# Kernel optimization log

Hardware: AMD Instinct MI355X
Metric: run time of the kernel (lower is better)

The kernel has to match this reference:

```python
import jax, jax.numpy as jnp
import numpy as np

H, NH, HD = 1024, 16, 64
WIN = 256
W = WIN // 2  # one-sided window
EXP = 4
PAD_VAL = 0.0  # pad_token_id
B, S0 = 2, 2048
NEG = float(np.finfo(np.float32).min)


def setup_inputs() -> dict:
    key = jax.random.key(0)
    ks = jax.random.split(key, 12)

    def lin(k, fi, fo):
        k1, k2 = jax.random.split(k)
        w = jax.random.normal(k1, (fi, fo), jnp.float32) / np.float32(np.sqrt(fi))
        b = jax.random.normal(k2, (fo,), jnp.float32) * 0.02
        return w, b

    x = jax.random.normal(ks[0], (B, S0, H), jnp.float32)
    mask = jnp.zeros((B, S0), jnp.int32)  # 0 = real token, 1 = pad
    wq, bq = lin(ks[1], H, H)
    wk, bk = lin(ks[2], H, H)
    wv, bv = lin(ks[3], H, H)
    wqg, bqg = lin(ks[4], H, H)
    wkg, bkg = lin(ks[5], H, H)
    wvg, bvg = lin(ks[6], H, H)
    ln_g = jnp.ones((H,), jnp.float32)
    ln_b = jnp.zeros((H,), jnp.float32)
    w1, b1 = lin(ks[7], H, H * EXP)
    w2, b2 = lin(ks[8], H * EXP, H)
    return dict(x=x, mask=mask, wq=wq, bq=bq, wk=wk, bk=bk, wv=wv, bv=bv,
                wqg=wqg, bqg=bqg, wkg=wkg, bkg=bkg, wvg=wvg, bvg=bvg,
                ln_g=ln_g, ln_b=ln_b, w1=w1, b1=b1, w2=w2, b2=b2)


def _forward(x, mask, wq, bq, wk, bk, wv, bv, wqg, bqg, wkg, bkg, wvg, bvg,
             ln_g, ln_b, w1, b1, w2, b2):
    Bsz, s0, _ = x.shape
    pad = WIN - s0 % WIN
    xp = jnp.pad(x, ((0, 0), (0, pad), (0, 0)), constant_values=PAD_VAL)
    m = jnp.pad(mask, ((0, 0), (0, pad)), constant_values=1)
    S = s0 + pad
    lm = (m * -10000).at[:, -1].set(10000)  # [B,S]; task='cls': last token global
    is_masked = lm < 0
    remove = lm != 0  # masked OR global keys removed from local windows

    inv_sqrt = np.float32(1.0 / np.sqrt(HD))
    q = ((xp @ wq + bq) * inv_sqrt).reshape(Bsz, S, NH, HD)
    k = (xp @ wk + bk).reshape(Bsz, S, NH, HD)
    v = (xp @ wv + bv).reshape(Bsz, S, NH, HD)

    nc = S // W
    # chunked banded scores: query chunk of W attends to 3W keys (prev/self/next)
    qc = q.transpose(0, 2, 1, 3).reshape(Bsz, NH, nc, W, HD)
    kpad = jnp.pad(k.transpose(0, 2, 1, 3), ((0, 0), (0, 0), (W, W), (0, 0)))
    idx3w = jnp.arange(nc)[:, None] * W + jnp.arange(3 * W)[None, :]  # [nc,3W]
    kc = kpad[:, :, idx3w]  # [B,NH,nc,3W,HD]
    sc = jnp.einsum('bhcpd,bhckd->bhcpk', qc, kc)  # [B,NH,nc,W,3W]
    p_idx = jnp.arange(W)[:, None]
    d_idx = jnp.arange(2 * W + 1)[None, :]
    band = sc[:, :, :, p_idx, p_idx + d_idx]  # [B,NH,nc,W,2W+1]
    band = band.reshape(Bsz, NH, S, 2 * W + 1).transpose(0, 2, 1, 3)  # [B,S,NH,2W+1]

    # key index j = i + d - W for offset d in [0, 2W]
    j = jnp.arange(S)[:, None] + jnp.arange(2 * W + 1)[None, :] - W
    in_range = (j >= 0) & (j < S)
    jc = jnp.clip(j, 0, S - 1)
    fmask = jnp.where(remove, NEG, 0.0)  # [B,S]
    band = band + fmask[:, jc][:, :, None, :]
    band = jnp.where(in_range[None, :, None, :], band, -jnp.inf)

    # global key column (single global token = last position), concatenated in front
    gcol = jnp.einsum('bshd,bhd->bsh', q, k[:, -1])[..., None]  # [B,S,NH,1]
    scores = jnp.concatenate([gcol, band], axis=-1)  # [B,S,NH,2W+2]
    probs = jax.nn.softmax(scores, axis=-1)
    probs = jnp.where(is_masked[:, :, None, None], 0.0, probs)

    out_g = probs[..., 0][..., None] * v[:, -1][:, None]  # [B,S,NH,HD]
    lp = probs[..., 1:].transpose(0, 2, 1, 3).reshape(Bsz, NH, nc, W, 2 * W + 1)
    pc = jnp.zeros((Bsz, NH, nc, W, 3 * W), probs.dtype).at[:, :, :, p_idx, p_idx + d_idx].set(lp)
    vpad = jnp.pad(v.transpose(0, 2, 1, 3), ((0, 0), (0, 0), (W, W), (0, 0)))
    vc = vpad[:, :, idx3w]  # [B,NH,nc,3W,HD]
    out_l = jnp.einsum('bhcpk,bhckd->bhcpd', pc, vc).reshape(Bsz, NH, S, HD).transpose(0, 2, 1, 3)
    attn = (out_l + out_g).reshape(Bsz, S, H)

    # full global attention for the global token (separate projections)
    qg = ((xp[:, -1] @ wqg + bqg) * inv_sqrt).reshape(Bsz, NH, HD)
    kg = (xp @ wkg + bkg).reshape(Bsz, S, NH, HD)
    vg = (xp @ wvg + bvg).reshape(Bsz, S, NH, HD)
    gs = jnp.einsum('bhd,bshd->bhs', qg, kg)
    gs = jnp.where(is_masked[:, None, :], NEG, gs)
    gout = jnp.einsum('bhs,bshd->bhd', jax.nn.softmax(gs, axis=-1), vg).reshape(Bsz, H)
    attn = attn.at[:, -1].set(gout)

    y = (xp + attn)[:, :s0]  # residual then strip padding
    mu = y.mean(-1, keepdims=True)
    var = ((y - mu) ** 2).mean(-1, keepdims=True)
    y = (y - mu) * jax.lax.rsqrt(var + 1e-5) * ln_g + ln_b
    h = jax.nn.gelu(y @ w1 + b1, approximate=False)
    return y + (h @ w2 + b2)


def reference(x, mask, wq, bq, wk, bk, wv, bv, wqg, bqg, wkg, bkg, wvg, bvg,
              ln_g, ln_b, w1, b1, w2, b2):
    return _forward(x, mask, wq, bq, wk, bk, wv, bv, wqg, bqg, wkg, bkg,
                    wvg, bvg, ln_g, ln_b, w1, b1, w2, b2)
```

## Files before the change

kernel.cpp:

```cpp
#include <hip/hip_runtime.h>


using bf16x8 = __attribute__((ext_vector_type(8))) short;
using bf16x4 = __attribute__((ext_vector_type(4))) short;
using f32x4  = __attribute__((ext_vector_type(4))) float;

__device__ __forceinline__ float b2f(short s) {
    return __uint_as_float(((unsigned int)(unsigned short)s) << 16);
}
__device__ __forceinline__ short f2b(float f) {
    unsigned int u = __float_as_uint(f);
    u += 0x7fffu + ((u >> 16) & 1u);
    return (short)(u >> 16);
}
__device__ __forceinline__ f32x4 mfma16(bf16x8 a, bf16x8 b, f32x4 c) {
    return __builtin_amdgcn_mfma_f32_16x16x32_bf16(a, b, c, 0, 0, 0);
}
__device__ __forceinline__ float safe_exp(float x) {
    return expf((x <= 0.f) ? x : 0.f);
}
__device__ __forceinline__ void load_lds16(const short* g, short* l) {
    __builtin_amdgcn_global_load_lds((const __attribute__((address_space(1))) void*)g,
                                     (__attribute__((address_space(3))) void*)l, 16, 0, 0);
}
#define NEGF (-3.0e38f)

__global__ void cvt_f32_bf16(const float* __restrict__ in, short* __restrict__ out, int n) {
    int i = (blockIdx.x * 256 + threadIdx.x) * 4;
    f32x4 v = *(const f32x4*)(in + i);
    bf16x4 o;
#pragma unroll
    for (int j = 0; j < 4; ++j) o[j] = f2b(v[j]);
    *(bf16x4*)(out + i) = o;
}

__global__ void cvt_transpose(const float* __restrict__ in, short* __restrict__ out,
                              int R, int C) {
    __shared__ short tile[32][33];
    int bx = blockIdx.x * 32, by = blockIdx.y * 32;
    int tx = threadIdx.x, ty = threadIdx.y;
    for (int i = ty; i < 32; i += 8)
        tile[i][tx] = f2b(in[(size_t)(by + i) * C + bx + tx]);
    __syncthreads();
    for (int i = ty; i < 32; i += 8)
        out[(size_t)(bx + i) * R + by + tx] = tile[tx][i];
}

__global__ void cvt_transpose_qkv(const float* __restrict__ wq, const float* __restrict__ wk,
                                  const float* __restrict__ wv, short* __restrict__ out) {
    __shared__ short tile[32][33];
    const float* in = (blockIdx.z == 0) ? wq : (blockIdx.z == 1) ? wk : wv;
    short* dst = out + (size_t)blockIdx.z * 1024 * 1024;
    int bx = blockIdx.x * 32, by = blockIdx.y * 32;
    int tx = threadIdx.x, ty = threadIdx.y;
    for (int i = ty; i < 32; i += 8)
        tile[i][tx] = f2b(in[(size_t)(by + i) * 1024 + bx + tx]);
    __syncthreads();
    for (int i = ty; i < 32; i += 8)
        dst[(size_t)(bx + i) * 1024 + by + tx] = tile[tx][i];
}

__global__ __launch_bounds__(256, 3) void gemm_bt(
    const short* __restrict__ A, const short* __restrict__ Bt,
    const float* __restrict__ bias0, const float* __restrict__ bias1,
    const float* __restrict__ bias2,
    short* __restrict__ C, short* __restrict__ Vt,
    int M, int N, int K, float scale, int mode)
{
    __shared__ short As[128 * 64];
    __shared__ short Bs[128 * 64];
    int m0 = blockIdx.x * 128, n0 = blockIdx.y * 128;
    int t = threadIdx.x;
    int wave = t >> 6, lane = t & 63, quad = lane >> 4, l16 = lane & 15;
    int wr = (wave >> 1) * 64, wc = (wave & 1) * 64;

    const short* ap[4]; const short* bp[4]; short* la[4]; short* lb[4];
    int gk = (((lane & 7) ^ (lane >> 3)) * 8);
#pragma unroll
    for (int l = 0; l < 4; ++l) {
        int c = wave * 4 + l;
        int row = c * 8 + (lane >> 3);
        ap[l] = A  + (size_t)(m0 + row) * K + gk;
        bp[l] = Bt + (size_t)(n0 + row) * K + gk;
        la[l] = As + c * 512;
        lb[l] = Bs + c * 512;
    }
    int sw = l16 & 7;

    f32x4 acc[4][4] = {};
    for (int k0 = 0; k0 < K; k0 += 64) {
#pragma unroll
        for (int l = 0; l < 4; ++l) { load_lds16(ap[l] + k0, la[l]); load_lds16(bp[l] + k0, lb[l]); }
        __syncthreads();
#pragma unroll
        for (int ks = 0; ks < 2; ++ks) {
            int slot = ((ks * 4 + quad) ^ sw) * 8;
            bf16x8 af[4], bfr[4];
#pragma unroll
            for (int i = 0; i < 4; ++i)
                af[i] = *(bf16x8*)(As + (wr + i * 16 + l16) * 64 + slot);
#pragma unroll
            for (int j = 0; j < 4; ++j)
                bfr[j] = *(bf16x8*)(Bs + (wc + j * 16 + l16) * 64 + slot);
#pragma unroll
            for (int i = 0; i < 4; ++i)
#pragma unroll
                for (int j = 0; j < 4; ++j)
                    acc[i][j] = mfma16(af[i], bfr[j], acc[i][j]);
        }
        __syncthreads();
    }

#pragma unroll
    for (int j = 0; j < 4; ++j) {
        int col = n0 + wc + j * 16 + l16;
        if (mode == 1) {
            float bs = bias0[col];
#pragma unroll
            for (int i = 0; i < 4; ++i) {
#pragma unroll
                for (int r = 0; r < 4; ++r) {
                    int row = m0 + wr + i * 16 + quad * 4 + r;
                    float v = acc[i][j][r] + bs;
                    v = 0.5f * v * (1.0f + erff(v * 0.70710678118f));
                    C[(size_t)row * N + col] = f2b(v);
                }
            }
        } else {
            int seg = col >> 10;
            const float* bpt = (seg == 0) ? bias0 : (seg == 1) ? bias1 : bias2;
            float bs = bpt[col & 1023];
            if (seg < 2) {
                float sc = (seg == 0) ? scale : 1.0f;
#pragma unroll
                for (int i = 0; i < 4; ++i)
#pragma unroll
                    for (int r = 0; r < 4; ++r) {
                        int row = m0 + wr + i * 16 + quad * 4 + r;
                        C[(size_t)row * N + col] = f2b((acc[i][j][r] + bs) * sc);
                    }
            } else {
                int h = (col >> 6) & 15, d = col & 63;
#pragma unroll
                for (int i = 0; i < 4; ++i) {
                    int row0 = m0 + wr + i * 16 + quad * 4;
                    int bb = row0 >> 11, s0 = row0 & 2047;
                    bf16x4 vv;
#pragma unroll
                    for (int r = 0; r < 4; ++r) vv[r] = f2b(acc[i][j][r] + bs);
                    *(bf16x4*)(Vt + (((size_t)(bb * 16 + h)) * 64 + d) * 2048 + s0) = vv;
                }
            }
        }
    }
}

__global__ __launch_bounds__(256, 4) void gemm64_bt(
    const short* __restrict__ A, const short* __restrict__ Bt,
    const float* __restrict__ bias, const float* __restrict__ resf,
    float* __restrict__ Cf, int M, int N, int K)
{
    __shared__ short As[64 * 64];
    __shared__ short Bs[64 * 64];
    int m0 = blockIdx.x * 64, n0 = blockIdx.y * 64;
    int t = threadIdx.x;
    int wave = t >> 6, lane = t & 63, quad = lane >> 4, l16 = lane & 15;
    int wr = (wave >> 1) * 32, wc = (wave & 1) * 32;

    const short* ap[2]; const short* bp[2]; short* la[2]; short* lb[2];
    int gk = (((lane & 7) ^ (lane >> 3)) * 8);
#pragma unroll
    for (int l = 0; l < 2; ++l) {
        int c = wave * 2 + l;
        int row = c * 8 + (lane >> 3);
        ap[l] = A  + (size_t)(m0 + row) * K + gk;
        bp[l] = Bt + (size_t)(n0 + row) * K + gk;
        la[l] = As + c * 512;
        lb[l] = Bs + c * 512;
    }
    int sw = l16 & 7;

    f32x4 acc[2][2] = {};
    for (int k0 = 0; k0 < K; k0 += 64) {
#pragma unroll
        for (int l = 0; l < 2; ++l) { load_lds16(ap[l] + k0, la[l]); load_lds16(bp[l] + k0, lb[l]); }
        __syncthreads();
#pragma unroll
        for (int ks = 0; ks < 2; ++ks) {
            int slot = ((ks * 4 + quad) ^ sw) * 8;
            bf16x8 af[2], bfr[2];
#pragma unroll
            for (int i = 0; i < 2; ++i)
                af[i] = *(bf16x8*)(As + (wr + i * 16 + l16) * 64 + slot);
#pragma unroll
            for (int j = 0; j < 2; ++j)
                bfr[j] = *(bf16x8*)(Bs + (wc + j * 16 + l16) * 64 + slot);
#pragma unroll
            for (int i = 0; i < 2; ++i)
#pragma unroll
                for (int j = 0; j < 2; ++j)
                    acc[i][j] = mfma16(af[i], bfr[j], acc[i][j]);
        }
        __syncthreads();
    }
#pragma unroll
    for (int j = 0; j < 2; ++j) {
        int col = n0 + wc + j * 16 + l16;
        float bs = bias[col];
#pragma unroll
        for (int i = 0; i < 2; ++i) {
#pragma unroll
            for (int r = 0; r < 4; ++r) {
                int row = m0 + wr + i * 16 + quad * 4 + r;
                Cf[(size_t)row * N + col] = acc[i][j][r] + bs + resf[(size_t)row * N + col];
            }
        }
    }
}

__global__ __launch_bounds__(256, 2) void attn_kernel(
    const short* __restrict__ QKV, const short* __restrict__ Vt,
    const int* __restrict__ mask,
    const float* __restrict__ bk, const float* __restrict__ bv,
    short* __restrict__ attn)
{
    extern __shared__ char smem[];
    short* PsQ = (short*)smem;
    short* KV  = (short*)(smem + 34816);
    float* gkf = (float*)(smem + 53248);
    float* gvf = (float*)(smem + 53504);

    int blk = blockIdx.x;
    int c = blk & 15, h = (blk >> 4) & 15, b = blk >> 8;
    int t = threadIdx.x;
    int wave = t >> 6, lane = t & 63, quad = lane >> 4, l16 = lane & 15;
    int q0 = c * 128;
    const int bs_off = b * 2048;
    const short* Q = QKV + h * 64;
    const short* K = QKV + 1024 + h * 64;

#pragma unroll
    for (int l = 0; l < 4; ++l) {
        int idx = l * 256 + t;
        int p = idx >> 3, dc = (idx & 7) * 8;
        *(bf16x8*)(PsQ + p * 72 + dc) =
            *(const bf16x8*)(Q + ((size_t)(bs_off + q0 + p)) * 3072 + dc);
    }
    if (t < 64) { gkf[t] = bk[h * 64 + t]; gvf[t] = bv[h * 64 + t]; }
    __syncthreads();

    bf16x8 aq[2][2];
#pragma unroll
    for (int ti = 0; ti < 2; ++ti)
#pragma unroll
        for (int ks = 0; ks < 2; ++ks)
            aq[ti][ks] = *(bf16x8*)(PsQ + (wave * 32 + ti * 16 + l16) * 72 + ks * 32 + quad * 8);

    float s_g[2][4];
#pragma unroll
    for (int ti = 0; ti < 2; ++ti)
#pragma unroll
        for (int r = 0; r < 4; ++r) {
            int row = wave * 32 + ti * 16 + quad * 4 + r;
            float part = 0.f;
#pragma unroll
            for (int dd = 0; dd < 4; ++dd) {
                int d = l16 * 4 + dd;
                part += b2f(PsQ[row * 72 + d]) * gkf[d];
            }
#pragma unroll
            for (int dsh = 1; dsh < 16; dsh <<= 1) part += __shfl_xor(part, dsh);
            s_g[ti][r] = part;
        }

    f32x4 o_acc[2][4] = {};
    float m_run[2][4], l_run[2][4];
#pragma unroll
    for (int ti = 0; ti < 2; ++ti)
#pragma unroll
        for (int r = 0; r < 4; ++r) { m_run[ti][r] = NEGF; l_run[ti][r] = 0.f; }

    int kt_beg = (q0 == 0) ? 1 : 0;
    int kt_end = (q0 + 256 > 2048) ? 2 : 3;
    for (int kt = kt_beg; kt < kt_end; ++kt) {
        int jb = q0 + (kt - 1) * 128;
        __syncthreads();
#pragma unroll
        for (int l = 0; l < 4; ++l) {
            int idx = l * 256 + t;
            int p = idx >> 3, dc = (idx & 7) * 8;
            *(bf16x8*)(KV + p * 72 + dc) =
                *(const bf16x8*)(K + ((size_t)(bs_off + jb + p)) * 3072 + dc);
        }
        __syncthreads();

        f32x4 s_acc[2][8] = {};
#pragma unroll
        for (int ks = 0; ks < 2; ++ks) {
            bf16x8 bk8[8];
#pragma unroll
            for (int tj = 0; tj < 8; ++tj)
                bk8[tj] = *(bf16x8*)(KV + (tj * 16 + l16) * 72 + ks * 32 + quad * 8);
#pragma unroll
            for (int ti = 0; ti < 2; ++ti)
#pragma unroll
                for (int tj = 0; tj < 8; ++tj)
                    s_acc[ti][tj] = mfma16(aq[ti][ks], bk8[tj], s_acc[ti][tj]);
        }

        float negj[8]; int jcol[8];
#pragma unroll
        for (int tj = 0; tj < 8; ++tj) {
            jcol[tj] = jb + tj * 16 + l16;
            negj[tj] = (mask[bs_off + jcol[tj]] != 0) ? NEGF : 0.f;
        }
        float tmax[2][4];
#pragma unroll
        for (int ti = 0; ti < 2; ++ti)
#pragma unroll
            for (int r = 0; r < 4; ++r) tmax[ti][r] = NEGF;
#pragma unroll
        for (int ti = 0; ti < 2; ++ti) {
            int irow_base = q0 + wave * 32 + ti * 16 + quad * 4;
#pragma unroll
            for (int tj = 0; tj < 8; ++tj)
#pragma unroll
                for (int r = 0; r < 4; ++r) {
                    int dj = jcol[tj] - (irow_base + r);
                    float sc = (dj >= -128 && dj <= 128) ? (s_acc[ti][tj][r] + negj[tj]) : NEGF;
                    s_acc[ti][tj][r] = sc;
                    tmax[ti][r] = fmaxf(tmax[ti][r], sc);
                }
        }
#pragma unroll
        for (int ti = 0; ti < 2; ++ti)
#pragma unroll
            for (int r = 0; r < 4; ++r)
#pragma unroll
                for (int dsh = 1; dsh < 16; dsh <<= 1)
                    tmax[ti][r] = fmaxf(tmax[ti][r], __shfl_xor(tmax[ti][r], dsh));

        float alpha[2][4], lsum[2][4];
#pragma unroll
        for (int ti = 0; ti < 2; ++ti)
#pragma unroll
            for (int r = 0; r < 4; ++r) {
                float mnew = fmaxf(m_run[ti][r], tmax[ti][r]);
                alpha[ti][r] = safe_exp(m_run[ti][r] - mnew);
                m_run[ti][r] = mnew;
                lsum[ti][r] = 0.f;
            }
#pragma unroll
        for (int ti = 0; ti < 2; ++ti)
#pragma unroll
            for (int tj = 0; tj < 8; ++tj)
#pragma unroll
                for (int r = 0; r < 4; ++r) {
                    float p = safe_exp(s_acc[ti][tj][r] - m_run[ti][r]);
                    lsum[ti][r] += p;
                    PsQ[(wave * 32 + ti * 16 + quad * 4 + r) * 136 + tj * 16 + l16] = f2b(p);
                }
#pragma unroll
        for (int ti = 0; ti < 2; ++ti)
#pragma unroll
            for (int r = 0; r < 4; ++r) {
#pragma unroll
                for (int dsh = 1; dsh < 16; dsh <<= 1) lsum[ti][r] += __shfl_xor(lsum[ti][r], dsh);
                l_run[ti][r] = l_run[ti][r] * alpha[ti][r] + lsum[ti][r];
            }
#pragma unroll
        for (int ti = 0; ti < 2; ++ti)
#pragma unroll
            for (int dj = 0; dj < 4; ++dj)
#pragma unroll
                for (int r = 0; r < 4; ++r) o_acc[ti][dj][r] *= alpha[ti][r];

        __syncthreads();
#pragma unroll
        for (int l = 0; l < 4; ++l) {
            int idx = l * 256 + t;
            int d = idx >> 4, kc = (idx & 15) * 8;
            *(bf16x8*)(KV + d * 136 + kc) =
                *(const bf16x8*)(Vt + ((size_t)(b * 16 + h) * 64 + d) * 2048 + jb + kc);
        }
        __syncthreads();
#pragma unroll
        for (int ks = 0; ks < 4; ++ks) {
            bf16x8 ap[2], bv8[4];
#pragma unroll
            for (int ti = 0; ti < 2; ++ti)
                ap[ti] = *(bf16x8*)(PsQ + (wave * 32 + ti * 16 + l16) * 136 + ks * 32 + quad * 8);
#pragma unroll
            for (int dj = 0; dj < 4; ++dj)
                bv8[dj] = *(bf16x8*)(KV + (dj * 16 + l16) * 136 + ks * 32 + quad * 8);
#pragma unroll
            for (int ti = 0; ti < 2; ++ti)
#pragma unroll
                for (int dj = 0; dj < 4; ++dj)
                    o_acc[ti][dj] = mfma16(ap[ti], bv8[dj], o_acc[ti][dj]);
        }
    }

#pragma unroll
    for (int ti = 0; ti < 2; ++ti) {
        int irow_base = q0 + wave * 32 + ti * 16 + quad * 4;
#pragma unroll
        for (int r = 0; r < 4; ++r) {
            int i = irow_base + r;
            float m2 = fmaxf(m_run[ti][r], s_g[ti][r]);
            float pg = safe_exp(s_g[ti][r] - m2);
            float al = safe_exp(m_run[ti][r] - m2);
            float l2 = l_run[ti][r] * al + pg;
            float invl = 1.f / fmaxf(l2, 1e-30f);
            float qm = (mask[bs_off + i] > 0) ? 0.f : 1.f;
#pragma unroll
            for (int dj = 0; dj < 4; ++dj) {
                int d = dj * 16 + l16;
                float val = (o_acc[ti][dj][r] * al + pg * gvf[d]) * invl * qm;
                attn[((size_t)(bs_off + i)) * 1024 + h * 64 + d] = f2b(val);
            }
        }
    }
}

__global__ __launch_bounds__(256) void resid_ln(
    const float* __restrict__ x, const short* __restrict__ attn,
    const float* __restrict__ g, const float* __restrict__ be,
    short* __restrict__ yb, float* __restrict__ yf)
{
    int row = blockIdx.x, t = threadIdx.x;
    int lane = t & 63, wave = t >> 6;
    const size_t base = (size_t)row * 1024;
    float v[4]; float s = 0.f, s2 = 0.f;
#pragma unroll
    for (int i = 0; i < 4; ++i) {
        int c = i * 256 + t;
        float val = x[base + c] + b2f(attn[base + c]);
        v[i] = val; s += val; s2 += val * val;
    }
#pragma unroll
    for (int off = 32; off > 0; off >>= 1) { s += __shfl_xor(s, off); s2 += __shfl_xor(s2, off); }
    __shared__ float red[8];
    if (lane == 0) { red[wave] = s; red[4 + wave] = s2; }
    __syncthreads();
    s  = red[0] + red[1] + red[2] + red[3];
    s2 = red[4] + red[5] + red[6] + red[7];
    float mu  = s * (1.f / 1024.f);
    float var = s2 * (1.f / 1024.f) - mu * mu;
    float inv = rsqrtf(fmaxf(var, 0.f) + 1e-5f);
#pragma unroll
    for (int i = 0; i < 4; ++i) {
        int c = i * 256 + t;
        float o = (v[i] - mu) * inv * g[c] + be[c];
        yb[base + c] = f2b(o);
        yf[base + c] = o;
    }
}

static constexpr size_t MEG      = 1048576;
static constexpr size_t OFF_WQKV = 0;
static constexpr size_t OFF_W1T  = 3 * MEG;
static constexpr size_t OFF_W2T  = 7 * MEG;
static constexpr size_t OFF_XB   = 11 * MEG;
static constexpr size_t OFF_QKV  = 15 * MEG;
static constexpr size_t OFF_VT   = 27 * MEG;
static constexpr size_t OFF_ATT  = 31 * MEG;
static constexpr size_t OFF_YN   = 35 * MEG;
static constexpr size_t OFF_YF   = 39 * MEG;
static constexpr size_t OFF_H    = OFF_QKV;

extern "C" void kernel_launch(void* const* d_in, const int* in_sizes, int n_in,
                              void* d_out, int out_size, void* d_ws, size_t ws_size,
                              hipStream_t stream) {
    (void)in_sizes; (void)n_in; (void)out_size; (void)ws_size;
    const float* x    = (const float*)d_in[0];
    const int*   mask = (const int*)  d_in[1];
    const float* wq   = (const float*)d_in[2];
    const float* bq   = (const float*)d_in[3];
    const float* wk   = (const float*)d_in[4];
    const float* bk   = (const float*)d_in[5];
    const float* wv   = (const float*)d_in[6];
    const float* bv   = (const float*)d_in[7];
    const float* lng  = (const float*)d_in[14];
    const float* lnb  = (const float*)d_in[15];
    const float* w1   = (const float*)d_in[16];
    const float* b1   = (const float*)d_in[17];
    const float* w2   = (const float*)d_in[18];
    const float* b2   = (const float*)d_in[19];
    short* ws  = (short*)d_ws;
    float* out = (float*)d_out;

    dim3 tb(32, 8);
    cvt_transpose_qkv<<<dim3(32, 32, 3), tb, 0, stream>>>(wq, wk, wv, ws + OFF_WQKV);
    cvt_transpose<<<dim3(128, 32), tb, 0, stream>>>(w1, ws + OFF_W1T, 1024, 4096);
    cvt_transpose<<<dim3(32, 128), tb, 0, stream>>>(w2, ws + OFF_W2T, 4096, 1024);
    cvt_f32_bf16<<<4096, 256, 0, stream>>>(x, ws + OFF_XB, 4194304);

    gemm_bt<<<dim3(32, 24), 256, 0, stream>>>(ws + OFF_XB, ws + OFF_WQKV,
                                              bq, bk, bv,
                                              ws + OFF_QKV, ws + OFF_VT,
                                              4096, 3072, 1024, 0.125f, 0);

    attn_kernel<<<512, 256, 53760, stream>>>(ws + OFF_QKV, ws + OFF_VT,
                                             mask, bk, bv, ws + OFF_ATT);

    resid_ln<<<4096, 256, 0, stream>>>(x, ws + OFF_ATT, lng, lnb,
                                       ws + OFF_YN, (float*)(ws + OFF_YF));

    gemm_bt<<<dim3(32, 32), 256, 0, stream>>>(ws + OFF_YN, ws + OFF_W1T,
                                              b1, nullptr, nullptr,
                                              ws + OFF_H, nullptr,
                                              4096, 4096, 1024, 1.0f, 1);
    gemm64_bt<<<dim3(64, 16), 256, 0, stream>>>(ws + OFF_H, ws + OFF_W2T,
                                                b2, (const float*)(ws + OFF_YF),
                                                out, 4096, 1024, 4096);
}
```

Baseline: 336.3 us.

## Replace FFN down-projection GEMM with 128x128 triple-buffered pipelined kernel

The second FFN GEMM (4096x1024, K=4096) moves from 64x64 tiles with a load-sync-compute loop to 128x128 tiles with a three-stage LDS ring buffer. Global loads for tile k+2 are issued before computing tile k, with explicit vmcnt waits and raw barriers. This cuts A/B reloads and hides memory latency. The cost is only 256 blocks on a many-CU GPU, with higher register and LDS use (96KB) per block.

```diff
diff --git a/kernel.cpp b/kernel.cpp
--- a/kernel.cpp
+++ b/kernel.cpp
@@ -155,64 +155,86 @@
     }
 }
 
-__global__ __launch_bounds__(256, 4) void gemm64_bt(
+__global__ __launch_bounds__(256) void gemm128_pipe(
     const short* __restrict__ A, const short* __restrict__ Bt,
     const float* __restrict__ bias, const float* __restrict__ resf,
     float* __restrict__ Cf, int M, int N, int K)
 {
-    __shared__ short As[64 * 64];
-    __shared__ short Bs[64 * 64];
-    int m0 = blockIdx.x * 64, n0 = blockIdx.y * 64;
+    __shared__ short As[3][128 * 64];
+    __shared__ short Bs[3][128 * 64];
+    int m0 = blockIdx.x * 128, n0 = blockIdx.y * 128;
     int t = threadIdx.x;
     int wave = t >> 6, lane = t & 63, quad = lane >> 4, l16 = lane & 15;
-    int wr = (wave >> 1) * 32, wc = (wave & 1) * 32;
-
-    const short* ap[2]; const short* bp[2]; short* la[2]; short* lb[2];
+    int wr = (wave >> 1) * 64, wc = (wave & 1) * 64;
+
+    const short* ap[4]; const short* bp[4]; int lo[4];
     int gk = (((lane & 7) ^ (lane >> 3)) * 8);
 #pragma unroll
-    for (int l = 0; l < 2; ++l) {
-        int c = wave * 2 + l;
+    for (int l = 0; l < 4; ++l) {
+        int c = wave * 4 + l;
         int row = c * 8 + (lane >> 3);
         ap[l] = A  + (size_t)(m0 + row) * K + gk;
         bp[l] = Bt + (size_t)(n0 + row) * K + gk;
-        la[l] = As + c * 512;
-        lb[l] = Bs + c * 512;
+        lo[l] = c * 512;
     }
     int sw = l16 & 7;
 
-    f32x4 acc[2][2] = {};
-    for (int k0 = 0; k0 < K; k0 += 64) {
-#pragma unroll
-        for (int l = 0; l < 2; ++l) { load_lds16(ap[l] + k0, la[l]); load_lds16(bp[l] + k0, lb[l]); }
-        __syncthreads();
+    const int nt = K >> 6;
+#pragma unroll
+    for (int l = 0; l < 4; ++l) { load_lds16(ap[l], &As[0][lo[l]]); load_lds16(bp[l], &Bs[0][lo[l]]); }
+#pragma unroll
+    for (int l = 0; l < 4; ++l) { load_lds16(ap[l] + 64, &As[1][lo[l]]); load_lds16(bp[l] + 64, &Bs[1][lo[l]]); }
+
+    f32x4 acc[4][4] = {};
+    int cur = 0, nxt = 2;
+    for (int ti = 0; ti < nt; ++ti) {
+        if (ti + 2 < nt) {
+            int k0 = (ti + 2) << 6;
+#pragma unroll
+            for (int l = 0; l < 4; ++l) { load_lds16(ap[l] + k0, &As[nxt][lo[l]]); load_lds16(bp[l] + k0, &Bs[nxt][lo[l]]); }
+            asm volatile("s_waitcnt vmcnt(16)" ::: "memory");
+        } else if (ti + 1 < nt) {
+            asm volatile("s_waitcnt vmcnt(8)" ::: "memory");
+        } else {
+            asm volatile("s_waitcnt vmcnt(0)" ::: "memory");
+        }
+        __builtin_amdgcn_s_barrier();
+        asm volatile("" ::: "memory");
+
+        const short* as = &As[cur][0];
+        const short* bs = &Bs[cur][0];
 #pragma unroll
         for (int ks = 0; ks < 2; ++ks) {
             int slot = ((ks * 4 + quad) ^ sw) * 8;
-            bf16x8 af[2], bfr[2];
-#pragma unroll
-            for (int i = 0; i < 2; ++i)
-                af[i] = *(bf16x8*)(As + (wr + i * 16 + l16) * 64 + slot);
-#pragma unroll
-            for (int j = 0; j < 2; ++j)
-                bfr[j] = *(bf16x8*)(Bs + (wc + j * 16 + l16) * 64 + slot);
-#pragma unroll
-            for (int i = 0; i < 2; ++i)
-#pragma unroll
-                for (int j = 0; j < 2; ++j)
+            bf16x8 af[4], bfr[4];
+#pragma unroll
+            for (int i = 0; i < 4; ++i)
+                af[i] = *(bf16x8*)(as + (wr + i * 16 + l16) * 64 + slot);
+#pragma unroll
+            for (int j = 0; j < 4; ++j)
+                bfr[j] = *(bf16x8*)(bs + (wc + j * 16 + l16) * 64 + slot);
+#pragma unroll
+            for (int i = 0; i < 4; ++i)
+#pragma unroll
+                for (int j = 0; j < 4; ++j)
                     acc[i][j] = mfma16(af[i], bfr[j], acc[i][j]);
         }
-        __syncthreads();
-    }
-#pragma unroll
-    for (int j = 0; j < 2; ++j) {
+        asm volatile("" ::: "memory");
+        __builtin_amdgcn_s_barrier();
+        cur = (cur == 2) ? 0 : cur + 1;
+        nxt = (nxt == 2) ? 0 : nxt + 1;
+    }
+
+#pragma unroll
+    for (int j = 0; j < 4; ++j) {
         int col = n0 + wc + j * 16 + l16;
-        float bs = bias[col];
-#pragma unroll
-        for (int i = 0; i < 2; ++i) {
+        float bsv = bias[col];
+#pragma unroll
+        for (int i = 0; i < 4; ++i) {
 #pragma unroll
             for (int r = 0; r < 4; ++r) {
                 int row = m0 + wr + i * 16 + quad * 4 + r;
-                Cf[(size_t)row * N + col] = acc[i][j][r] + bs + resf[(size_t)row * N + col];
+                Cf[(size_t)row * N + col] = acc[i][j][r] + bsv + resf[(size_t)row * N + col];
             }
         }
     }
@@ -511,7 +533,7 @@
                                               b1, nullptr, nullptr,
                                               ws + OFF_H, nullptr,
                                               4096, 4096, 1024, 1.0f, 1);
-    gemm64_bt<<<dim3(64, 16), 256, 0, stream>>>(ws + OFF_H, ws + OFF_W2T,
-                                                b2, (const float*)(ws + OFF_YF),
-                                                out, 4096, 1024, 4096);
-}
+    gemm128_pipe<<<dim3(32, 8), 256, 0, stream>>>(ws + OFF_H, ws + OFF_W2T,
+                                                  b2, (const float*)(ws + OFF_YF),
+                                                  out, 4096, 1024, 4096);
+}
```

Result: slower. 354.3 us (+5.4%).

## Stage GEMM epilogue through LDS for coalesced stores; double-buffer FFN2 GEMM

Applied to the files above, without the earlier changes.

The 128x128 GEMM epilogue now writes results into a padded shared-memory tile and then emits 16-byte row-contiguous global stores. The V-transpose output goes through the same tile, so Vt is written with vectorized 8-element stores instead of scattered 4-element ones. The second FFN GEMM gains a double-buffered LDS pipeline: the next K-tile's global-to-LDS loads are issued before computing on the current tile, using explicit vmcnt waits and raw barriers. The larger shared-memory footprint may reduce occupancy, and the hand-written waitcnt logic depends on how many loads are in flight per thread.

```diff
diff --git a/kernel.cpp b/kernel.cpp
--- a/kernel.cpp
+++ b/kernel.cpp
@@ -67,8 +67,9 @@
     short* __restrict__ C, short* __restrict__ Vt,
     int M, int N, int K, float scale, int mode)
 {
-    __shared__ short As[128 * 64];
-    __shared__ short Bs[128 * 64];
+    __shared__ short sh[128 * 136];
+    short* As = sh;
+    short* Bs = sh + 8192;
     int m0 = blockIdx.x * 128, n0 = blockIdx.y * 128;
     int t = threadIdx.x;
     int wave = t >> 6, lane = t & 63, quad = lane >> 4, l16 = lane & 15;
@@ -111,63 +112,82 @@
         __syncthreads();
     }
 
-#pragma unroll
-    for (int j = 0; j < 4; ++j) {
-        int col = n0 + wc + j * 16 + l16;
+    int seg0 = n0 >> 10;
+    if (mode == 1 || seg0 < 2) {
         if (mode == 1) {
-            float bs = bias0[col];
-#pragma unroll
-            for (int i = 0; i < 4; ++i) {
-#pragma unroll
-                for (int r = 0; r < 4; ++r) {
-                    int row = m0 + wr + i * 16 + quad * 4 + r;
-                    float v = acc[i][j][r] + bs;
-                    v = 0.5f * v * (1.0f + erff(v * 0.70710678118f));
-                    C[(size_t)row * N + col] = f2b(v);
-                }
+#pragma unroll
+            for (int j = 0; j < 4; ++j) {
+                int col = n0 + wc + j * 16 + l16;
+                float bs = bias0[col];
+#pragma unroll
+                for (int i = 0; i < 4; ++i)
+#pragma unroll
+                    for (int r = 0; r < 4; ++r) {
+                        float v = acc[i][j][r] + bs;
+                        v = 0.5f * v * (1.0f + erff(v * 0.70710678118f));
+                        sh[(wr + i * 16 + quad * 4 + r) * 136 + wc + j * 16 + l16] = f2b(v);
+                    }
             }
         } else {
-            int seg = col >> 10;
-            const float* bpt = (seg == 0) ? bias0 : (seg == 1) ? bias1 : bias2;
-            float bs = bpt[col & 1023];
-            if (seg < 2) {
-                float sc = (seg == 0) ? scale : 1.0f;
+            float sc = (seg0 == 0) ? scale : 1.0f;
+            const float* bpt = (seg0 == 0) ? bias0 : bias1;
+#pragma unroll
+            for (int j = 0; j < 4; ++j) {
+                int col = n0 + wc + j * 16 + l16;
+                float bs = bpt[col & 1023];
 #pragma unroll
                 for (int i = 0; i < 4; ++i)
 #pragma unroll
-                    for (int r = 0; r < 4; ++r) {
-                        int row = m0 + wr + i * 16 + quad * 4 + r;
-                        C[(size_t)row * N + col] = f2b((acc[i][j][r] + bs) * sc);
-                    }
-            } else {
-                int h = (col >> 6) & 15, d = col & 63;
-#pragma unroll
-                for (int i = 0; i < 4; ++i) {
-                    int row0 = m0 + wr + i * 16 + quad * 4;
-                    int bb = row0 >> 11, s0 = row0 & 2047;
-                    bf16x4 vv;
-#pragma unroll
-                    for (int r = 0; r < 4; ++r) vv[r] = f2b(acc[i][j][r] + bs);
-                    *(bf16x4*)(Vt + (((size_t)(bb * 16 + h)) * 64 + d) * 2048 + s0) = vv;
-                }
-            }
-        }
-    }
-}
-
-__global__ __launch_bounds__(256, 4) void gemm64_bt(
+                    for (int r = 0; r < 4; ++r)
+                        sh[(wr + i * 16 + quad * 4 + r) * 136 + wc + j * 16 + l16] =
+                            f2b((acc[i][j][r] + bs) * sc);
+            }
+        }
+        __syncthreads();
+        int row = t >> 1, half = t & 1;
+        const short* src = sh + row * 136 + half * 64;
+        short* dst = C + (size_t)(m0 + row) * N + n0 + half * 64;
+#pragma unroll
+        for (int cgk = 0; cgk < 8; ++cgk)
+            *(bf16x8*)(dst + cgk * 8) = *(const bf16x8*)(src + cgk * 8);
+    } else {
+#pragma unroll
+        for (int j = 0; j < 4; ++j) {
+            int cl = wc + j * 16 + l16;
+            float bs = bias2[(n0 & 1023) + cl];
+#pragma unroll
+            for (int i = 0; i < 4; ++i)
+#pragma unroll
+                for (int r = 0; r < 4; ++r)
+                    sh[cl * 136 + wr + i * 16 + quad * 4 + r] = f2b(acc[i][j][r] + bs);
+        }
+        __syncthreads();
+        int h0 = (n0 & 1023) >> 6;
+        int bb = m0 >> 11, s0 = m0 & 2047;
+        int sc = t & 15;
+#pragma unroll
+        for (int cgk = 0; cgk < 8; ++cgk) {
+            int cl = (t >> 4) + cgk * 16;
+            int h = h0 + (cl >> 6), d = cl & 63;
+            *(bf16x8*)(Vt + (((size_t)(bb * 16 + h)) * 64 + d) * 2048 + s0 + sc * 8) =
+                *(const bf16x8*)(sh + cl * 136 + sc * 8);
+        }
+    }
+}
+
+__global__ __launch_bounds__(256, 4) void gemm64_db(
     const short* __restrict__ A, const short* __restrict__ Bt,
     const float* __restrict__ bias, const float* __restrict__ resf,
     float* __restrict__ Cf, int M, int N, int K)
 {
-    __shared__ short As[64 * 64];
-    __shared__ short Bs[64 * 64];
+    __shared__ short As[2][64 * 64];
+    __shared__ short Bs[2][64 * 64];
     int m0 = blockIdx.x * 64, n0 = blockIdx.y * 64;
     int t = threadIdx.x;
     int wave = t >> 6, lane = t & 63, quad = lane >> 4, l16 = lane & 15;
     int wr = (wave >> 1) * 32, wc = (wave & 1) * 32;
 
-    const short* ap[2]; const short* bp[2]; short* la[2]; short* lb[2];
+    const short* ap[2]; const short* bp[2]; int lo[2];
     int gk = (((lane & 7) ^ (lane >> 3)) * 8);
 #pragma unroll
     for (int l = 0; l < 2; ++l) {
@@ -175,34 +195,53 @@
         int row = c * 8 + (lane >> 3);
         ap[l] = A  + (size_t)(m0 + row) * K + gk;
         bp[l] = Bt + (size_t)(n0 + row) * K + gk;
-        la[l] = As + c * 512;
-        lb[l] = Bs + c * 512;
+        lo[l] = c * 512;
     }
     int sw = l16 & 7;
 
+    const int nt = K >> 6;
+#pragma unroll
+    for (int l = 0; l < 2; ++l) { load_lds16(ap[l], &As[0][lo[l]]); load_lds16(bp[l], &Bs[0][lo[l]]); }
+
     f32x4 acc[2][2] = {};
-    for (int k0 = 0; k0 < K; k0 += 64) {
-#pragma unroll
-        for (int l = 0; l < 2; ++l) { load_lds16(ap[l] + k0, la[l]); load_lds16(bp[l] + k0, lb[l]); }
-        __syncthreads();
+    for (int ti = 0; ti < nt; ++ti) {
+        int cur = ti & 1;
+        if (ti + 1 < nt) {
+            int k0 = (ti + 1) << 6;
+#pragma unroll
+            for (int l = 0; l < 2; ++l) {
+                load_lds16(ap[l] + k0, &As[cur ^ 1][lo[l]]);
+                load_lds16(bp[l] + k0, &Bs[cur ^ 1][lo[l]]);
+            }
+            asm volatile("s_waitcnt vmcnt(4)" ::: "memory");
+        } else {
+            asm volatile("s_waitcnt vmcnt(0)" ::: "memory");
+        }
+        __builtin_amdgcn_s_barrier();
+        asm volatile("" ::: "memory");
+
+        const short* as = &As[cur][0];
+        const short* bs = &Bs[cur][0];
 #pragma unroll
         for (int ks = 0; ks < 2; ++ks) {
             int slot = ((ks * 4 + quad) ^ sw) * 8;
             bf16x8 af[2], bfr[2];
 #pragma unroll
             for (int i = 0; i < 2; ++i)
-                af[i] = *(bf16x8*)(As + (wr + i * 16 + l16) * 64 + slot);
+                af[i] = *(bf16x8*)(as + (wr + i * 16 + l16) * 64 + slot);
 #pragma unroll
             for (int j = 0; j < 2; ++j)
-                bfr[j] = *(bf16x8*)(Bs + (wc + j * 16 + l16) * 64 + slot);
+                bfr[j] = *(bf16x8*)(bs + (wc + j * 16 + l16) * 64 + slot);
 #pragma unroll
             for (int i = 0; i < 2; ++i)
 #pragma unroll
                 for (int j = 0; j < 2; ++j)
                     acc[i][j] = mfma16(af[i], bfr[j], acc[i][j]);
         }
-        __syncthreads();
-    }
+        asm volatile("" ::: "memory");
+        __builtin_amdgcn_s_barrier();
+    }
+
 #pragma unroll
     for (int j = 0; j < 2; ++j) {
         int col = n0 + wc + j * 16 + l16;
@@ -511,7 +550,7 @@
                                               b1, nullptr, nullptr,
                                               ws + OFF_H, nullptr,
                                               4096, 4096, 1024, 1.0f, 1);
-    gemm64_bt<<<dim3(64, 16), 256, 0, stream>>>(ws + OFF_H, ws + OFF_W2T,
+    gemm64_db<<<dim3(64, 16), 256, 0, stream>>>(ws + OFF_H, ws + OFF_W2T,
                                                 b2, (const float*)(ws + OFF_YF),
                                                 out, 4096, 1024, 4096);
 }
```

New measurement: 354.1 us. 1.05x slower.
